# Kernel optimization log

Hardware: AMD Instinct MI355X
Metric: run time of the kernel (lower is better)

The kernel has to match this reference:

```python
import jax, jax.numpy as jnp
import numpy as np

POOLED_H, POOLED_W = 7, 7
SPATIAL_SCALE = 0.25
SAMPLING_RATIO = 2
N, C, H, W = 2, 256, 200, 200
K = 1000
IMG = 800.0  # image-space extent (H/spatial_scale)


def setup_inputs() -> dict:
    key = jax.random.key(0)
    k1, k2, k3 = jax.random.split(key, 3)
    inp = jax.random.normal(k1, (N, C, H, W), dtype=jnp.float32)
    # boxes in image coordinates (x1,y1,x2,y2) with x1<=x2, y1<=y2
    pts = jax.random.uniform(k2, (K, 2, 2), dtype=jnp.float32) * (IMG - 1.0)  # [K,2,(x,y)]
    lo = jnp.min(pts, axis=1)  # [K,2] -> x1,y1
    hi = jnp.max(pts, axis=1)  # [K,2] -> x2,y2
    b = jax.random.randint(k3, (K,), 0, N).astype(jnp.float32)
    rois = jnp.concatenate([b[:, None], lo[:, :1], lo[:, 1:], hi[:, :1], hi[:, 1:]], axis=1)
    return {"input": inp, "rois": rois}


def _interp_axis(coord, size):
    """Per-axis bilinear setup (torchvision roi_align semantics).
    coord: [...], returns (low_idx, high_idx, low_w, high_w, valid)."""
    valid = (coord >= -1.0) & (coord <= size)
    c = jnp.clip(coord, 0.0, None)
    low = jnp.floor(c).astype(jnp.int32)
    over = low >= size - 1
    low = jnp.where(over, size - 1, low)
    high = jnp.where(over, size - 1, low + 1)
    frac = jnp.where(over, 0.0, c - low.astype(c.dtype))  # l (weight for high)
    return low, high, 1.0 - frac, frac, valid


def roi_align_fwd(input, rois):
    Nn, Cc, Hh, Ww = input.shape
    sr = SAMPLING_RATIO
    b = rois[:, 0].astype(jnp.int32)                       # [K]
    x1, y1, x2, y2 = [rois[:, i] * SPATIAL_SCALE for i in (1, 2, 3, 4)]
    roi_w = jnp.maximum(x2 - x1, 1.0)
    roi_h = jnp.maximum(y2 - y1, 1.0)
    bin_h = roi_h / POOLED_H
    bin_w = roi_w / POOLED_W

    ph = jnp.arange(POOLED_H, dtype=jnp.float32)
    pw = jnp.arange(POOLED_W, dtype=jnp.float32)
    off = (jnp.arange(sr, dtype=jnp.float32) + 0.5) / sr
    # sample coordinates: [K, PH*sr] and [K, PW*sr]
    ys = (y1[:, None, None] + (ph[None, :, None] + off[None, None, :]) * bin_h[:, None, None]).reshape(rois.shape[0], POOLED_H * sr)
    xs = (x1[:, None, None] + (pw[None, :, None] + off[None, None, :]) * bin_w[:, None, None]).reshape(rois.shape[0], POOLED_W * sr)

    yl, yh, wyl, wyh, vy = _interp_axis(ys, Hh)
    xl, xh, wxl, wxh, vx = _interp_axis(xs, Ww)

    bi = b[:, None, None]

    def gather(yi, xi):  # -> [K, Gy, Gx, C]
        return input[bi, :, yi[:, :, None], xi[:, None, :]]

    val = (
        (wyl[:, :, None] * wxl[:, None, :])[..., None] * gather(yl, xl)
        + (wyl[:, :, None] * wxh[:, None, :])[..., None] * gather(yl, xh)
        + (wyh[:, :, None] * wxl[:, None, :])[..., None] * gather(yh, xl)
        + (wyh[:, :, None] * wxh[:, None, :])[..., None] * gather(yh, xh)
    )  # [K, Gy, Gx, C]
    mask = (vy[:, :, None] & vx[:, None, :]).astype(val.dtype)[..., None]
    val = val * mask
    Kk = rois.shape[0]
    out = val.reshape(Kk, POOLED_H, sr, POOLED_W, sr, Cc).sum(axis=(2, 4)) / (sr * sr)
    return jnp.transpose(out, (0, 3, 1, 2))  # [K, C, PH, PW]


def reference(input, rois):
    return roi_align_fwd(input, rois)
```

## Files before the change

### kernel.cpp

```cpp
#include <hip/hip_runtime.h>
#include <hip/hip_bf16.h>

constexpr int Nn = 2, Cc = 256, Hh = 200, Ww = 200, Kk = 1000;
constexpr int PH = 7, PW = 7, SR = 2;
constexpr float SCALE = 0.25f;
constexpr int HWsz = Hh * Ww;

__global__ __launch_bounds__(256) void transpose_to_nhwc_bf16(
    const float* __restrict__ in, __hip_bfloat16* __restrict__ out) {
  __shared__ float tile[64][65];
  const int hw0 = blockIdx.x * 64;
  const int c0  = blockIdx.y * 64;
  const int b   = blockIdx.z;
  const int lane = threadIdx.x & 63;
  const int row  = threadIdx.x >> 6;

#pragma unroll
  for (int i = 0; i < 16; ++i) {
    const int cc = row + i * 4;
    tile[cc][lane] = in[(size_t)(b * Cc + c0 + cc) * HWsz + hw0 + lane];
  }
  __syncthreads();
#pragma unroll
  for (int i = 0; i < 16; ++i) {
    const int hh = row + i * 4;
    out[((size_t)b * HWsz + hw0 + hh) * Cc + c0 + lane] =
        __float2bfloat16(tile[lane][hh]);
  }
}

__device__ __forceinline__ int sidx(int c, int p) {
  return c * 49 + p + 13 * (c >> 2);
}

__global__ __launch_bounds__(448, 2) void roi_align_nhwc_bf16(
    const ushort* __restrict__ feat, const float* __restrict__ rois,
    float* __restrict__ out) {
  __shared__ float stage[6704];

  const int k    = blockIdx.x;
  const int half = blockIdx.y;
  const int ph   = (int)(threadIdx.x >> 6);
  const int lane = (int)(threadIdx.x & 63);
  const int ixl  = lane >> 5;
  const int cq   = lane & 31;

  const float* r = rois + k * 5;
  const int b = (int)r[0];
  const float x1 = r[1] * SCALE;
  const float y1 = r[2] * SCALE;
  const float x2 = r[3] * SCALE;
  const float y2 = r[4] * SCALE;
  const float bin_w = fmaxf(x2 - x1, 1.0f) * (1.0f / PW);
  const float bin_h = fmaxf(y2 - y1, 1.0f) * (1.0f / PH);

  const ushort4* fb =
      (const ushort4*)(feat + (size_t)b * HWsz * Cc) + half * 32 + cq;

  float4 acc[PW];
#pragma unroll
  for (int i = 0; i < PW; ++i) acc[i] = make_float4(0.f, 0.f, 0.f, 0.f);

  auto bf2f = [](ushort u) -> float {
    return __uint_as_float((unsigned)u << 16);
  };

  const float x_off = ((float)ixl + 0.5f) * 0.5f;

#pragma unroll
  for (int iy = 0; iy < SR; ++iy) {
    const float y  = y1 + ((float)ph + ((float)iy + 0.5f) * 0.5f) * bin_h;
    const bool vy  = (y >= -1.0f) && (y <= (float)Hh);
    const float cy = fmaxf(y, 0.0f);
    int yl = (int)cy;
    int yh;
    float fy;
    if (yl >= Hh - 1) { yl = Hh - 1; yh = Hh - 1; fy = 0.0f; }
    else              { yh = yl + 1; fy = cy - (float)yl; }
    float wyl = 1.0f - fy, wyh = fy;
    if (!vy) { wyl = 0.0f; wyh = 0.0f; }
    const int ylb = yl * Ww, yhb = yh * Ww;

    ushort4 v00[PW], v01[PW], v10[PW], v11[PW];
#pragma unroll
    for (int pw = 0; pw < PW; ++pw) {
      const float x  = x1 + ((float)pw + x_off) * bin_w;
      const float cx = fmaxf(x, 0.0f);
      int xl = (int)cx;
      int xh;
      if (xl >= Ww - 1) { xl = Ww - 1; xh = Ww - 1; }
      else              { xh = xl + 1; }
      v00[pw] = fb[(ylb + xl) * 64];
      v01[pw] = fb[(ylb + xh) * 64];
      v10[pw] = fb[(yhb + xl) * 64];
      v11[pw] = fb[(yhb + xh) * 64];
    }

    __builtin_amdgcn_sched_barrier(0);

#pragma unroll
    for (int pw = 0; pw < PW; ++pw) {
      const float x  = x1 + ((float)pw + x_off) * bin_w;
      const bool vx  = (x >= -1.0f) && (x <= (float)Ww);
      const float cx = fmaxf(x, 0.0f);
      const int xl = (int)cx;
      float fx;
      if (xl >= Ww - 1) { fx = 0.0f; }
      else              { fx = cx - (float)xl; }
      float wxl = 1.0f - fx, wxh = fx;
      if (!vx) { wxl = 0.0f; wxh = 0.0f; }

      const float w00 = wyl * wxl, w01 = wyl * wxh;
      const float w10 = wyh * wxl, w11 = wyh * wxh;

      acc[pw].x = fmaf(w00, bf2f(v00[pw].x), fmaf(w01, bf2f(v01[pw].x),
                  fmaf(w10, bf2f(v10[pw].x), fmaf(w11, bf2f(v11[pw].x), acc[pw].x))));
      acc[pw].y = fmaf(w00, bf2f(v00[pw].y), fmaf(w01, bf2f(v01[pw].y),
                  fmaf(w10, bf2f(v10[pw].y), fmaf(w11, bf2f(v11[pw].y), acc[pw].y))));
      acc[pw].z = fmaf(w00, bf2f(v00[pw].z), fmaf(w01, bf2f(v01[pw].z),
                  fmaf(w10, bf2f(v10[pw].z), fmaf(w11, bf2f(v11[pw].z), acc[pw].z))));
      acc[pw].w = fmaf(w00, bf2f(v00[pw].w), fmaf(w01, bf2f(v01[pw].w),
                  fmaf(w10, bf2f(v10[pw].w), fmaf(w11, bf2f(v11[pw].w), acc[pw].w))));
    }
  }

#pragma unroll
  for (int pw = 0; pw < PW; ++pw) {
    acc[pw].x += __shfl_xor(acc[pw].x, 32);
    acc[pw].y += __shfl_xor(acc[pw].y, 32);
    acc[pw].z += __shfl_xor(acc[pw].z, 32);
    acc[pw].w += __shfl_xor(acc[pw].w, 32);
  }

  const float inv = 1.0f / (SR * SR);
  if (lane < 32) {
    const int c0 = cq * 4;
    const int p = ph * PW;
#pragma unroll
    for (int pw = 0; pw < PW; ++pw) {
      stage[sidx(c0 + 0, p + pw)] = acc[pw].x * inv;
      stage[sidx(c0 + 1, p + pw)] = acc[pw].y * inv;
      stage[sidx(c0 + 2, p + pw)] = acc[pw].z * inv;
      stage[sidx(c0 + 3, p + pw)] = acc[pw].w * inv;
    }
  }
  __syncthreads();

  const size_t obase = (size_t)k * (Cc * PH * PW) + (size_t)half * (128 * PH * PW);
#pragma unroll
  for (int i = 0; i < 14; ++i) {
    const int idx = i * 448 + (int)threadIdx.x;
    const int c = idx / 49, p = idx - c * 49;
    out[obase + idx] = stage[sidx(c, p)];
  }
}

extern "C" void kernel_launch(void* const* d_in, const int* in_sizes, int n_in,
                              void* d_out, int out_size, void* d_ws, size_t ws_size,
                              hipStream_t stream) {
  const float* inp  = (const float*)d_in[0];
  const float* rois = (const float*)d_in[1];
  float* out = (float*)d_out;

  __hip_bfloat16* nhwc = (__hip_bfloat16*)d_ws;
  transpose_to_nhwc_bf16<<<dim3(HWsz / 64, Cc / 64, Nn), 256, 0, stream>>>(inp, nhwc);
  roi_align_nhwc_bf16<<<dim3(Kk, 2), 448, 0, stream>>>((const ushort*)nhwc, rois, out);
}
```

Measured before the change: 78.01 us.

## Make ROI-align a persistent kernel with atomic work queue and nontemporal stores

Replaces the one-block-per-(ROI, channel-half) grid with 512 persistent blocks. Each block repeatedly grabs a unit from a global atomic counter, which is reset by a memset before launch. Output stores become nontemporal so the results do not pollute the cache. This aims to cut block launch and tail overhead, at the cost of an extra memset launch, one atomic per unit and extra barriers, while per-unit work is already nearly uniform.

```diff
diff --git a/kernel.cpp b/kernel.cpp
--- a/kernel.cpp
+++ b/kernel.cpp
@@ -5,6 +5,7 @@
 constexpr int PH = 7, PW = 7, SR = 2;
 constexpr float SCALE = 0.25f;
 constexpr int HWsz = Hh * Ww;
+constexpr unsigned NUNITS = 2 * Kk;
 
 __global__ __launch_bounds__(256) void transpose_to_nhwc_bf16(
     const float* __restrict__ in, __hip_bfloat16* __restrict__ out) {
@@ -33,125 +34,135 @@
   return c * 49 + p + 13 * (c >> 2);
 }
 
-__global__ __launch_bounds__(448, 2) void roi_align_nhwc_bf16(
+__global__ __launch_bounds__(448, 2) void roi_align_ws(
     const ushort* __restrict__ feat, const float* __restrict__ rois,
-    float* __restrict__ out) {
+    float* __restrict__ out, unsigned* __restrict__ counter) {
   __shared__ float stage[6704];
+  __shared__ unsigned s_unit;
 
-  const int k    = blockIdx.x;
-  const int half = blockIdx.y;
-  const int ph   = (int)(threadIdx.x >> 6);
-  const int lane = (int)(threadIdx.x & 63);
+  const int tid  = (int)threadIdx.x;
+  const int ph   = tid >> 6;
+  const int lane = tid & 63;
   const int ixl  = lane >> 5;
   const int cq   = lane & 31;
-
-  const float* r = rois + k * 5;
-  const int b = (int)r[0];
-  const float x1 = r[1] * SCALE;
-  const float y1 = r[2] * SCALE;
-  const float x2 = r[3] * SCALE;
-  const float y2 = r[4] * SCALE;
-  const float bin_w = fmaxf(x2 - x1, 1.0f) * (1.0f / PW);
-  const float bin_h = fmaxf(y2 - y1, 1.0f) * (1.0f / PH);
-
-  const ushort4* fb =
-      (const ushort4*)(feat + (size_t)b * HWsz * Cc) + half * 32 + cq;
-
-  float4 acc[PW];
-#pragma unroll
-  for (int i = 0; i < PW; ++i) acc[i] = make_float4(0.f, 0.f, 0.f, 0.f);
 
   auto bf2f = [](ushort u) -> float {
     return __uint_as_float((unsigned)u << 16);
   };
-
   const float x_off = ((float)ixl + 0.5f) * 0.5f;
 
+  for (;;) {
+    if (tid == 0) s_unit = atomicAdd(counter, 1u);
+    __syncthreads();
+    const unsigned unit = s_unit;
+    if (unit >= NUNITS) return;
+
+    const int k    = (int)(unit >> 1);
+    const int half = (int)(unit & 1);
+
+    const float* r = rois + k * 5;
+    const int b = (int)r[0];
+    const float x1 = r[1] * SCALE;
+    const float y1 = r[2] * SCALE;
+    const float x2 = r[3] * SCALE;
+    const float y2 = r[4] * SCALE;
+    const float bin_w = fmaxf(x2 - x1, 1.0f) * (1.0f / PW);
+    const float bin_h = fmaxf(y2 - y1, 1.0f) * (1.0f / PH);
+
+    const ushort4* fb =
+        (const ushort4*)(feat + (size_t)b * HWsz * Cc) + half * 32 + cq;
+
+    float4 acc[PW];
 #pragma unroll
-  for (int iy = 0; iy < SR; ++iy) {
-    const float y  = y1 + ((float)ph + ((float)iy + 0.5f) * 0.5f) * bin_h;
-    const bool vy  = (y >= -1.0f) && (y <= (float)Hh);
-    const float cy = fmaxf(y, 0.0f);
-    int yl = (int)cy;
-    int yh;
-    float fy;
-    if (yl >= Hh - 1) { yl = Hh - 1; yh = Hh - 1; fy = 0.0f; }
-    else              { yh = yl + 1; fy = cy - (float)yl; }
-    float wyl = 1.0f - fy, wyh = fy;
-    if (!vy) { wyl = 0.0f; wyh = 0.0f; }
-    const int ylb = yl * Ww, yhb = yh * Ww;
+    for (int i = 0; i < PW; ++i) acc[i] = make_float4(0.f, 0.f, 0.f, 0.f);
 
-    ushort4 v00[PW], v01[PW], v10[PW], v11[PW];
 #pragma unroll
-    for (int pw = 0; pw < PW; ++pw) {
-      const float x  = x1 + ((float)pw + x_off) * bin_w;
-      const float cx = fmaxf(x, 0.0f);
-      int xl = (int)cx;
-      int xh;
-      if (xl >= Ww - 1) { xl = Ww - 1; xh = Ww - 1; }
-      else              { xh = xl + 1; }
-      v00[pw] = fb[(ylb + xl) * 64];
-      v01[pw] = fb[(ylb + xh) * 64];
-      v10[pw] = fb[(yhb + xl) * 64];
-      v11[pw] = fb[(yhb + xh) * 64];
+    for (int iy = 0; iy < SR; ++iy) {
+      const float y  = y1 + ((float)ph + ((float)iy + 0.5f) * 0.5f) * bin_h;
+      const bool vy  = (y >= -1.0f) && (y <= (float)Hh);
+      const float cy = fmaxf(y, 0.0f);
+      int yl = (int)cy;
+      int yh;
+      float fy;
+      if (yl >= Hh - 1) { yl = Hh - 1; yh = Hh - 1; fy = 0.0f; }
+      else              { yh = yl + 1; fy = cy - (float)yl; }
+      float wyl = 1.0f - fy, wyh = fy;
+      if (!vy) { wyl = 0.0f; wyh = 0.0f; }
+      const int ylb = yl * Ww, yhb = yh * Ww;
+
+      ushort4 v00[PW], v01[PW], v10[PW], v11[PW];
+#pragma unroll
+      for (int pw = 0; pw < PW; ++pw) {
+        const float x  = x1 + ((float)pw + x_off) * bin_w;
+        const float cx = fmaxf(x, 0.0f);
+        int xl = (int)cx;
+        int xh;
+        if (xl >= Ww - 1) { xl = Ww - 1; xh = Ww - 1; }
+        else              { xh = xl + 1; }
+        v00[pw] = fb[(ylb + xl) * 64];
+        v01[pw] = fb[(ylb + xh) * 64];
+        v10[pw] = fb[(yhb + xl) * 64];
+        v11[pw] = fb[(yhb + xh) * 64];
+      }
+
+      __builtin_amdgcn_sched_barrier(0);
+
+#pragma unroll
+      for (int pw = 0; pw < PW; ++pw) {
+        const float x  = x1 + ((float)pw + x_off) * bin_w;
+        const bool vx  = (x >= -1.0f) && (x <= (float)Ww);
+        const float cx = fmaxf(x, 0.0f);
+        const int xl = (int)cx;
+        float fx;
+        if (xl >= Ww - 1) { fx = 0.0f; }
+        else              { fx = cx - (float)xl; }
+        float wxl = 1.0f - fx, wxh = fx;
+        if (!vx) { wxl = 0.0f; wxh = 0.0f; }
+
+        const float w00 = wyl * wxl, w01 = wyl * wxh;
+        const float w10 = wyh * wxl, w11 = wyh * wxh;
+
+        acc[pw].x = fmaf(w00, bf2f(v00[pw].x), fmaf(w01, bf2f(v01[pw].x),
+                    fmaf(w10, bf2f(v10[pw].x), fmaf(w11, bf2f(v11[pw].x), acc[pw].x))));
+        acc[pw].y = fmaf(w00, bf2f(v00[pw].y), fmaf(w01, bf2f(v01[pw].y),
+                    fmaf(w10, bf2f(v10[pw].y), fmaf(w11, bf2f(v11[pw].y), acc[pw].y))));
+        acc[pw].z = fmaf(w00, bf2f(v00[pw].z), fmaf(w01, bf2f(v01[pw].z),
+                    fmaf(w10, bf2f(v10[pw].z), fmaf(w11, bf2f(v11[pw].z), acc[pw].z))));
+        acc[pw].w = fmaf(w00, bf2f(v00[pw].w), fmaf(w01, bf2f(v01[pw].w),
+                    fmaf(w10, bf2f(v10[pw].w), fmaf(w11, bf2f(v11[pw].w), acc[pw].w))));
+      }
     }
-
-    __builtin_amdgcn_sched_barrier(0);
 
 #pragma unroll
     for (int pw = 0; pw < PW; ++pw) {
-      const float x  = x1 + ((float)pw + x_off) * bin_w;
-      const bool vx  = (x >= -1.0f) && (x <= (float)Ww);
-      const float cx = fmaxf(x, 0.0f);
-      const int xl = (int)cx;
-      float fx;
-      if (xl >= Ww - 1) { fx = 0.0f; }
-      else              { fx = cx - (float)xl; }
-      float wxl = 1.0f - fx, wxh = fx;
-      if (!vx) { wxl = 0.0f; wxh = 0.0f; }
+      acc[pw].x += __shfl_xor(acc[pw].x, 32);
+      acc[pw].y += __shfl_xor(acc[pw].y, 32);
+      acc[pw].z += __shfl_xor(acc[pw].z, 32);
+      acc[pw].w += __shfl_xor(acc[pw].w, 32);
+    }
 
-      const float w00 = wyl * wxl, w01 = wyl * wxh;
-      const float w10 = wyh * wxl, w11 = wyh * wxh;
+    const float inv = 1.0f / (SR * SR);
+    if (lane < 32) {
+      const int c0 = cq * 4;
+      const int p = ph * PW;
+#pragma unroll
+      for (int pw = 0; pw < PW; ++pw) {
+        stage[sidx(c0 + 0, p + pw)] = acc[pw].x * inv;
+        stage[sidx(c0 + 1, p + pw)] = acc[pw].y * inv;
+        stage[sidx(c0 + 2, p + pw)] = acc[pw].z * inv;
+        stage[sidx(c0 + 3, p + pw)] = acc[pw].w * inv;
+      }
+    }
+    __syncthreads();
 
-      acc[pw].x = fmaf(w00, bf2f(v00[pw].x), fmaf(w01, bf2f(v01[pw].x),
-                  fmaf(w10, bf2f(v10[pw].x), fmaf(w11, bf2f(v11[pw].x), acc[pw].x))));
-      acc[pw].y = fmaf(w00, bf2f(v00[pw].y), fmaf(w01, bf2f(v01[pw].y),
-                  fmaf(w10, bf2f(v10[pw].y), fmaf(w11, bf2f(v11[pw].y), acc[pw].y))));
-      acc[pw].z = fmaf(w00, bf2f(v00[pw].z), fmaf(w01, bf2f(v01[pw].z),
-                  fmaf(w10, bf2f(v10[pw].z), fmaf(w11, bf2f(v11[pw].z), acc[pw].z))));
-      acc[pw].w = fmaf(w00, bf2f(v00[pw].w), fmaf(w01, bf2f(v01[pw].w),
-                  fmaf(w10, bf2f(v10[pw].w), fmaf(w11, bf2f(v11[pw].w), acc[pw].w))));
+    const size_t obase =
+        (size_t)k * (Cc * PH * PW) + (size_t)half * (128 * PH * PW);
+#pragma unroll
+    for (int i = 0; i < 14; ++i) {
+      const int idx = i * 448 + tid;
+      const int c = idx / 49, p = idx - c * 49;
+      __builtin_nontemporal_store(stage[sidx(c, p)], &out[obase + idx]);
     }
-  }
-
-#pragma unroll
-  for (int pw = 0; pw < PW; ++pw) {
-    acc[pw].x += __shfl_xor(acc[pw].x, 32);
-    acc[pw].y += __shfl_xor(acc[pw].y, 32);
-    acc[pw].z += __shfl_xor(acc[pw].z, 32);
-    acc[pw].w += __shfl_xor(acc[pw].w, 32);
-  }
-
-  const float inv = 1.0f / (SR * SR);
-  if (lane < 32) {
-    const int c0 = cq * 4;
-    const int p = ph * PW;
-#pragma unroll
-    for (int pw = 0; pw < PW; ++pw) {
-      stage[sidx(c0 + 0, p + pw)] = acc[pw].x * inv;
-      stage[sidx(c0 + 1, p + pw)] = acc[pw].y * inv;
-      stage[sidx(c0 + 2, p + pw)] = acc[pw].z * inv;
-      stage[sidx(c0 + 3, p + pw)] = acc[pw].w * inv;
-    }
-  }
-  __syncthreads();
-
-  const size_t obase = (size_t)k * (Cc * PH * PW) + (size_t)half * (128 * PH * PW);
-#pragma unroll
-  for (int i = 0; i < 14; ++i) {
-    const int idx = i * 448 + (int)threadIdx.x;
-    const int c = idx / 49, p = idx - c * 49;
-    out[obase + idx] = stage[sidx(c, p)];
   }
 }
 
@@ -163,6 +174,9 @@
   float* out = (float*)d_out;
 
   __hip_bfloat16* nhwc = (__hip_bfloat16*)d_ws;
+  unsigned* counter = (unsigned*)((char*)d_ws + (48u << 20));
+
   transpose_to_nhwc_bf16<<<dim3(HWsz / 64, Cc / 64, Nn), 256, 0, stream>>>(inp, nhwc);
-  roi_align_nhwc_bf16<<<dim3(Kk, 2), 448, 0, stream>>>((const ushort*)nhwc, rois, out);
+  hipMemsetAsync(counter, 0, sizeof(unsigned), stream);
+  roi_align_ws<<<dim3(512), 448, 0, stream>>>((const ushort*)nhwc, rois, out, counter);
 }
```

New measurement: 78.78 us. No clear change (+1.0%).
